# Kernel optimization log

Hardware: AMD Instinct MI355X
Metric: run time of the kernel (lower is better)

## Reference

```python
import jax, jax.numpy as jnp
import numpy as np

LN_EPS = 1e-5
NEG_SLOPE = 0.01

def layer_norm(h, gamma, beta):
    mu = jnp.mean(h, axis=-1, keepdims=True)
    var = jnp.var(h, axis=-1, keepdims=True)
    return (h - mu) * jax.lax.rsqrt(var + LN_EPS) * gamma + beta

def setup_inputs() -> dict:
    key = jax.random.key(0)
    ks = jax.random.split(key, 12)
    N, E = 50000, 600000
    D_NODE, D_EDGE, D_IN = 128, 64, 192  # D_IN = D_NODE + D_EDGE
    x = jax.random.normal(ks[0], (N, D_NODE), dtype=jnp.float32)
    edge_index = jax.random.randint(ks[1], (2, E), 0, N, dtype=jnp.int64)
    edge_attr = jax.random.normal(ks[2], (E, D_EDGE), dtype=jnp.float32)
    # mlp_before_agg: Linear(192->128) + LayerNorm + LeakyReLU
    W1 = jax.random.normal(ks[3], (D_IN, D_NODE), dtype=jnp.float32) / np.sqrt(D_IN)
    b1 = jnp.zeros((D_NODE,), dtype=jnp.float32)
    g1 = jnp.ones((D_NODE,), dtype=jnp.float32)
    be1 = jnp.zeros((D_NODE,), dtype=jnp.float32)
    # mlp_after_agg: Linear(128->128) + LayerNorm + LeakyReLU
    W2 = jax.random.normal(ks[4], (D_NODE, D_NODE), dtype=jnp.float32) / np.sqrt(D_NODE)
    b2 = jnp.zeros((D_NODE,), dtype=jnp.float32)
    g2 = jnp.ones((D_NODE,), dtype=jnp.float32)
    be2 = jnp.zeros((D_NODE,), dtype=jnp.float32)
    return {"x": x, "edge_index": edge_index, "edge_attr": edge_attr,
            "W1": W1, "b1": b1, "g1": g1, "be1": be1,
            "W2": W2, "b2": b2, "g2": g2, "be2": be2}

def reference(x, edge_index, edge_attr, W1, b1, g1, be1, W2, b2, g2, be2):
    N = x.shape[0]
    row, col = edge_index[0], edge_index[1]
    # 1. gather + concat: (E, D_NODE + D_EDGE)
    out = jnp.concatenate([x[row], edge_attr], axis=1)
    # 2. pre-agg MLP: Linear + LayerNorm + LeakyReLU
    out = jax.nn.leaky_relu(layer_norm(out @ W1 + b1, g1, be1), NEG_SLOPE)
    # 3. scatter-mean aggregate over destination nodes (empty segments -> 0)
    sums = jax.ops.segment_sum(out, col, num_segments=N)
    counts = jax.ops.segment_sum(jnp.ones((out.shape[0], 1), out.dtype), col, num_segments=N)
    out = sums / jnp.maximum(counts, 1.0)
    # 4. post-agg MLP + residual + activation
    out = jax.nn.leaky_relu(layer_norm(out @ W2 + b2, g2, be2), NEG_SLOPE)
    return jax.nn.leaky_relu(out + x, NEG_SLOPE)
```

## Files before the change

kernel.cpp:

```cpp
#include <hip/hip_runtime.h>

#define D_NODE 128
#define D_EDGE 64
#define D_IN   192
#define NEG    0.01f
#define LN_EPS 1e-5f

typedef short bf16x8 __attribute__((ext_vector_type(8)));
typedef float f32x4  __attribute__((ext_vector_type(4)));

__device__ __forceinline__ unsigned f2bf(float f) {
    unsigned u = __builtin_bit_cast(unsigned, f);
    return (u + 0x7FFFu + ((u >> 16) & 1u)) >> 16;
}
__device__ __forceinline__ unsigned pk2(float a, float b) {
    return f2bf(a) | (f2bf(b) << 16);
}
__device__ __forceinline__ float bf2f(unsigned short s) {
    unsigned u = ((unsigned)s) << 16;
    return __builtin_bit_cast(float, u);
}

__global__ void k_hist(const int* __restrict__ ei, int* __restrict__ hist, int E) {
    int i = blockIdx.x * blockDim.x + threadIdx.x;
    int stride = gridDim.x * blockDim.x;
    for (int e = i; e < E; e += stride) atomicAdd(&hist[ei[E + e]], 1);
}

__global__ __launch_bounds__(1024) void k_scanA(const int* __restrict__ hist,
                                                int* __restrict__ base,
                                                int* __restrict__ blockTot, int N) {
    __shared__ int wsum[16], woff[16];
    const int t = threadIdx.x, b = blockIdx.x;
    const int i = b * 1024 + t;
    const int lane = t & 63, w = t >> 6;
    int v = (i < N) ? hist[i] : 0;
    int x = v;
    #pragma unroll
    for (int d = 1; d < 64; d <<= 1) { int u = __shfl_up(x, d); if (lane >= d) x += u; }
    if (lane == 63) wsum[w] = x;
    __syncthreads();
    if (t < 16) {
        int y = wsum[t];
        #pragma unroll
        for (int d = 1; d < 16; d <<= 1) { int u = __shfl_up(y, d, 16); if (t >= d) y += u; }
        woff[t] = y - wsum[t];
    }
    __syncthreads();
    int incl = x + woff[w];
    if (i < N) base[i] = incl - v;
    if (t == 1023) blockTot[b] = incl;
}

__global__ void k_scanB(int* __restrict__ blockTot, int NB) {
    int t = threadIdx.x;
    int v = (t < NB) ? blockTot[t] : 0;
    int x = v;
    #pragma unroll
    for (int d = 1; d < 64; d <<= 1) { int u = __shfl_up(x, d); if (t >= d) x += u; }
    if (t < NB) blockTot[t] = x - v;
}

__global__ __launch_bounds__(1024) void k_scanC(int* __restrict__ base,
                                                const int* __restrict__ blockTot, int N) {
    int i = blockIdx.x * 1024 + threadIdx.x;
    if (i < N) base[i] += blockTot[blockIdx.x];
}

__global__ void k_bucket(const int* __restrict__ ei, int* __restrict__ base,
                         int* __restrict__ perm, int* __restrict__ srcrow,
                         int* __restrict__ dstcol, int E) {
    int i = blockIdx.x * blockDim.x + threadIdx.x;
    int stride = gridDim.x * blockDim.x;
    for (int e = i; e < E; e += stride) {
        int c = ei[E + e];
        int r = ei[e];
        int p = atomicAdd(&base[c], 1);
        perm[p]   = e;
        srcrow[p] = r;
        dstcol[p] = c;
    }
}

__global__ __launch_bounds__(256) void edge_mfma_seg(
    const float* __restrict__ x,
    const float* __restrict__ edge_attr,
    const int*   __restrict__ perm,
    const int*   __restrict__ srcrow,
    const int*   __restrict__ dstcol,
    const float* __restrict__ W1,
    const float* __restrict__ b1,
    const float* __restrict__ g1,
    const float* __restrict__ be1,
    float* __restrict__ sums,
    int E, int ntiles)
{
    __shared__ unsigned short h[64][200];
    __shared__ float rS [64][4], rS2[64][4];
    __shared__ int   scol[64];
    __shared__ unsigned long long maskSh;

    const int tid = threadIdx.x;
    const int w   = tid >> 6;
    const int l   = tid & 63;
    const int lm  = l & 15;
    const int q   = l >> 4;
    const int q8  = q * 8;

    bf16x8 Bfr[2][6];
    float  b1v[2], g1v[2], bev[2];
    #pragma unroll
    for (int c2 = 0; c2 < 2; ++c2) {
        const int n = (2 * w + c2) * 16 + lm;
        b1v[c2] = b1[n]; g1v[c2] = g1[n]; bev[c2] = be1[n];
        #pragma unroll
        for (int kt = 0; kt < 6; ++kt) {
            bf16x8 f;
            #pragma unroll
            for (int j = 0; j < 8; ++j)
                f[j] = (short)f2bf(W1[(kt * 32 + q8 + j) * 128 + n]);
            Bfr[c2][kt] = f;
        }
    }

    for (int tile = blockIdx.x; tile < ntiles; tile += gridDim.x) {
        const int e0 = tile * 64;

        {
            const int e  = tid >> 2;
            const int qq = tid & 3;
            const int ge = e0 + e;
            if (ge < E) {
                const int row = srcrow[ge];
                const int eid = perm[ge];
                const float4* xr = (const float4*)(x + (size_t)row * D_NODE);
                #pragma unroll
                for (int i = 0; i < 8; ++i) {
                    float4 v = xr[qq * 8 + i];
                    *(uint2*)&h[e][qq * 32 + i * 4] =
                        make_uint2(pk2(v.x, v.y), pk2(v.z, v.w));
                }
                const float4* ar = (const float4*)(edge_attr + (size_t)eid * D_EDGE);
                #pragma unroll
                for (int i = 0; i < 4; ++i) {
                    float4 v = ar[qq * 4 + i];
                    *(uint2*)&h[e][128 + qq * 16 + i * 4] =
                        make_uint2(pk2(v.x, v.y), pk2(v.z, v.w));
                }
            } else {
                #pragma unroll
                for (int i = 0; i < 8; ++i)
                    *(uint2*)&h[e][qq * 32 + i * 4] = make_uint2(0u, 0u);
                #pragma unroll
                for (int i = 0; i < 4; ++i)
                    *(uint2*)&h[e][128 + qq * 16 + i * 4] = make_uint2(0u, 0u);
            }
            if (tid < 64)
                scol[tid] = (e0 + tid < E) ? dstcol[e0 + tid] : -1;
        }
        __syncthreads();

        f32x4 acc[4][2];
        #pragma unroll
        for (int et = 0; et < 4; ++et)
            #pragma unroll
            for (int c2 = 0; c2 < 2; ++c2)
                acc[et][c2] = (f32x4){0.f, 0.f, 0.f, 0.f};

        #pragma unroll
        for (int et = 0; et < 4; ++et) {
            bf16x8 Afr[6];
            #pragma unroll
            for (int kt = 0; kt < 6; ++kt)
                Afr[kt] = *(const bf16x8*)&h[et * 16 + lm][kt * 32 + q8];
            #pragma unroll
            for (int c2 = 0; c2 < 2; ++c2)
                #pragma unroll
                for (int kt = 0; kt < 6; ++kt)
                    acc[et][c2] = __builtin_amdgcn_mfma_f32_16x16x32_bf16(
                        Afr[kt], Bfr[c2][kt], acc[et][c2], 0, 0, 0);
        }

        #pragma unroll
        for (int et = 0; et < 4; ++et) {
            #pragma unroll
            for (int r = 0; r < 4; ++r) {
                float v0 = acc[et][0][r] + b1v[0];
                float v1 = acc[et][1][r] + b1v[1];
                acc[et][0][r] = v0;
                acc[et][1][r] = v1;
                float s  = v0 + v1;
                float s2 = v0 * v0 + v1 * v1;
                #pragma unroll
                for (int off = 1; off < 16; off <<= 1) {
                    s  += __shfl_xor(s,  off, 16);
                    s2 += __shfl_xor(s2, off, 16);
                }
                if (lm == 0) {
                    const int em = et * 16 + q * 4 + r;
                    rS [em][w] = s;
                    rS2[em][w] = s2;
                }
            }
        }
        __syncthreads();

        if (tid < 64) {
            int me = scol[tid];
            int pv = (tid == 0) ? (me ^ 1) : scol[tid - 1];
            unsigned long long m = __ballot(me != pv);
            if (tid == 0) maskSh = m;
        }

        #pragma unroll
        for (int et = 0; et < 4; ++et) {
            #pragma unroll
            for (int r = 0; r < 4; ++r) {
                const int em = et * 16 + q * 4 + r;
                float4 p  = *(const float4*)&rS [em][0];
                float4 p2 = *(const float4*)&rS2[em][0];
                const float S    = (p.x  + p.y)  + (p.z  + p.w);
                const float S2   = (p2.x + p2.y) + (p2.z + p2.w);
                const float mu   = S * (1.f / 128.f);
                const float var  = S2 * (1.f / 128.f) - mu * mu;
                const float rstd = rsqrtf(var + LN_EPS);
                #pragma unroll
                for (int c2 = 0; c2 < 2; ++c2) {
                    float y = (acc[et][c2][r] - mu) * rstd * g1v[c2] + bev[c2];
                    y = (y > 0.f) ? y : NEG * y;
                    h[em][(2 * w + c2) * 16 + lm] = (unsigned short)f2bf(y);
                }
            }
        }
        __syncthreads();

        {
            const unsigned long long mask = maskSh;
            const int g  = tid >> 7;
            const int j  = tid & 127;
            const int lo = g * 32, hi = lo + 32;
            float s = 0.f;
            int rs = lo;
            for (int em = lo; em < hi; ++em) {
                s += bf2f(h[em][j]);
                const int nx = em + 1;
                const bool isEnd = (nx == hi) || ((mask >> nx) & 1ull);
                if (isEnd) {
                    const int dest = scol[em];
                    if (dest >= 0) {
                        const bool sg = (rs > 0) && ((mask >> rs) & 1ull);
                        const bool eg = (em < 63) && ((mask >> nx) & 1ull);
                        float* p = &sums[(size_t)dest * D_NODE + j];
                        if (sg && eg) *p = s;
                        else          atomicAdd(p, s);
                    }
                    s = 0.f; rs = nx;
                }
            }
        }
        __syncthreads();
    }
}

__global__ __launch_bounds__(256) void node_mfma(
    const float* __restrict__ sums,
    const int*   __restrict__ hist,
    const float* __restrict__ x,
    const float* __restrict__ W2,
    const float* __restrict__ b2,
    const float* __restrict__ g2,
    const float* __restrict__ be2,
    float* __restrict__ out,
    int N)
{
    __shared__ unsigned short h[64][136];
    __shared__ float rS [64][4], rS2[64][4];

    const int tid = threadIdx.x;
    const int w   = tid >> 6;
    const int l   = tid & 63;
    const int lm  = l & 15;
    const int q   = l >> 4;
    const int q8  = q * 8;

    bf16x8 Bfr[2][4];
    float  b2v[2], g2v[2], bev[2];
    #pragma unroll
    for (int c2 = 0; c2 < 2; ++c2) {
        const int n = (2 * w + c2) * 16 + lm;
        b2v[c2] = b2[n]; g2v[c2] = g2[n]; bev[c2] = be2[n];
        #pragma unroll
        for (int kt = 0; kt < 4; ++kt) {
            bf16x8 f;
            #pragma unroll
            for (int j = 0; j < 8; ++j)
                f[j] = (short)f2bf(W2[(kt * 32 + q8 + j) * 128 + n]);
            Bfr[c2][kt] = f;
        }
    }

    const int n0 = blockIdx.x * 64;

    {
        const int e  = tid >> 2;
        const int qq = tid & 3;
        const int gn = n0 + e;
        if (gn < N) {
            const int cnt = hist[gn];
            const float sc = (cnt > 0) ? 1.f / (float)cnt : 0.f;
            const float4* sr = (const float4*)(sums + (size_t)gn * D_NODE);
            #pragma unroll
            for (int i = 0; i < 8; ++i) {
                float4 v = sr[qq * 8 + i];
                *(uint2*)&h[e][qq * 32 + i * 4] =
                    make_uint2(pk2(v.x * sc, v.y * sc), pk2(v.z * sc, v.w * sc));
            }
        } else {
            #pragma unroll
            for (int i = 0; i < 8; ++i)
                *(uint2*)&h[e][qq * 32 + i * 4] = make_uint2(0u, 0u);
        }
    }
    __syncthreads();

    f32x4 acc[4][2];
    #pragma unroll
    for (int et = 0; et < 4; ++et)
        #pragma unroll
        for (int c2 = 0; c2 < 2; ++c2)
            acc[et][c2] = (f32x4){0.f, 0.f, 0.f, 0.f};

    #pragma unroll
    for (int et = 0; et < 4; ++et) {
        bf16x8 Afr[4];
        #pragma unroll
        for (int kt = 0; kt < 4; ++kt)
            Afr[kt] = *(const bf16x8*)&h[et * 16 + lm][kt * 32 + q8];
        #pragma unroll
        for (int c2 = 0; c2 < 2; ++c2)
            #pragma unroll
            for (int kt = 0; kt < 4; ++kt)
                acc[et][c2] = __builtin_amdgcn_mfma_f32_16x16x32_bf16(
                    Afr[kt], Bfr[c2][kt], acc[et][c2], 0, 0, 0);
    }

    #pragma unroll
    for (int et = 0; et < 4; ++et) {
        #pragma unroll
        for (int r = 0; r < 4; ++r) {
            float v0 = acc[et][0][r] + b2v[0];
            float v1 = acc[et][1][r] + b2v[1];
            acc[et][0][r] = v0;
            acc[et][1][r] = v1;
            float s  = v0 + v1;
            float s2 = v0 * v0 + v1 * v1;
            #pragma unroll
            for (int off = 1; off < 16; off <<= 1) {
                s  += __shfl_xor(s,  off, 16);
                s2 += __shfl_xor(s2, off, 16);
            }
            if (lm == 0) {
                const int em = et * 16 + q * 4 + r;
                rS [em][w] = s;
                rS2[em][w] = s2;
            }
        }
    }
    __syncthreads();

    #pragma unroll
    for (int et = 0; et < 4; ++et) {
        #pragma unroll
        for (int r = 0; r < 4; ++r) {
            const int em = et * 16 + q * 4 + r;
            const int gn = n0 + em;
            if (gn >= N) continue;
            float4 p  = *(const float4*)&rS [em][0];
            float4 p2 = *(const float4*)&rS2[em][0];
            const float S    = (p.x  + p.y)  + (p.z  + p.w);
            const float S2   = (p2.x + p2.y) + (p2.z + p2.w);
            const float mu   = S * (1.f / 128.f);
            const float var  = S2 * (1.f / 128.f) - mu * mu;
            const float rstd = rsqrtf(var + LN_EPS);
            #pragma unroll
            for (int c2 = 0; c2 < 2; ++c2) {
                const int col = (2 * w + c2) * 16 + lm;
                float y = (acc[et][c2][r] - mu) * rstd * g2v[c2] + bev[c2];
                y = (y > 0.f) ? y : NEG * y;
                float rr = y + x[(size_t)gn * D_NODE + col];
                rr = (rr > 0.f) ? rr : NEG * rr;
                out[(size_t)gn * D_NODE + col] = rr;
            }
        }
    }
}

extern "C" void kernel_launch(void* const* d_in, const int* in_sizes, int n_in,
                              void* d_out, int out_size, void* d_ws, size_t ws_size,
                              hipStream_t stream) {
    const float* x          = (const float*)d_in[0];
    const int*   edge_index = (const int*)  d_in[1];
    const float* edge_attr  = (const float*)d_in[2];
    const float* W1         = (const float*)d_in[3];
    const float* b1         = (const float*)d_in[4];
    const float* g1         = (const float*)d_in[5];
    const float* be1        = (const float*)d_in[6];
    const float* W2         = (const float*)d_in[7];
    const float* b2         = (const float*)d_in[8];
    const float* g2         = (const float*)d_in[9];
    const float* be2        = (const float*)d_in[10];

    const int N = in_sizes[0] / D_NODE;
    const int E = in_sizes[1] / 2;

    float* sums     = (float*)d_ws;
    int*   hist     = (int*)(sums + (size_t)N * D_NODE);
    int*   base     = hist + N;
    int*   blockTot = base + N;
    int*   perm     = blockTot + 64;
    int*   srcrow   = perm + E;
    int*   dstcol   = srcrow + E;

    hipMemsetAsync(d_ws, 0, ((size_t)N * D_NODE + (size_t)N) * sizeof(float), stream);

    k_hist<<<dim3(256), dim3(256), 0, stream>>>(edge_index, hist, E);
    const int NB = (N + 1023) / 1024;
    k_scanA<<<dim3(NB), dim3(1024), 0, stream>>>(hist, base, blockTot, N);
    k_scanB<<<dim3(1),  dim3(64),   0, stream>>>(blockTot, NB);
    k_scanC<<<dim3(NB), dim3(1024), 0, stream>>>(base, blockTot, N);
    k_bucket<<<dim3(256), dim3(256), 0, stream>>>(edge_index, base, perm, srcrow, dstcol, E);

    const int ntiles = (E + 63) / 64;
    const int grid   = ntiles < 1280 ? ntiles : 1280;
    edge_mfma_seg<<<dim3(grid), dim3(256), 0, stream>>>(
        x, edge_attr, perm, srcrow, dstcol, W1, b1, g1, be1, sums, E, ntiles);

    node_mfma<<<dim3((N + 63) / 64), dim3(256), 0, stream>>>(
        sums, hist, x, W2, b2, g2, be2, (float*)d_out, N);
}
```

Baseline: 509.7 us.

## Replace scan with atomic bucket allocation and pre-swizzle MFMA operand layout in LDS

The three-kernel prefix scan is replaced by a single atomic cursor allocator that gives each destination node a contiguous slot range, in arbitrary node order. The bucket kernel now writes only the permutation, and the edge kernel reads source and destination indices indirectly through edge_index. Gathered edge features are stored in LDS in an MFMA-fragment-ready layout so each lane loads one contiguous vector. The LayerNorm output is written transposed, so the segmented reduction reads contiguous per-column data, and that loop is fully unrolled. These changes cut launches and global index traffic, at the cost of extra indirect loads and narrower float2 global reads.

```diff
diff --git a/kernel.cpp b/kernel.cpp
--- a/kernel.cpp
+++ b/kernel.cpp
@@ -27,58 +27,19 @@
     for (int e = i; e < E; e += stride) atomicAdd(&hist[ei[E + e]], 1);
 }
 
-__global__ __launch_bounds__(1024) void k_scanA(const int* __restrict__ hist,
-                                                int* __restrict__ base,
-                                                int* __restrict__ blockTot, int N) {
-    __shared__ int wsum[16], woff[16];
-    const int t = threadIdx.x, b = blockIdx.x;
-    const int i = b * 1024 + t;
-    const int lane = t & 63, w = t >> 6;
-    int v = (i < N) ? hist[i] : 0;
-    int x = v;
-    #pragma unroll
-    for (int d = 1; d < 64; d <<= 1) { int u = __shfl_up(x, d); if (lane >= d) x += u; }
-    if (lane == 63) wsum[w] = x;
-    __syncthreads();
-    if (t < 16) {
-        int y = wsum[t];
-        #pragma unroll
-        for (int d = 1; d < 16; d <<= 1) { int u = __shfl_up(y, d, 16); if (t >= d) y += u; }
-        woff[t] = y - wsum[t];
-    }
-    __syncthreads();
-    int incl = x + woff[w];
-    if (i < N) base[i] = incl - v;
-    if (t == 1023) blockTot[b] = incl;
-}
-
-__global__ void k_scanB(int* __restrict__ blockTot, int NB) {
-    int t = threadIdx.x;
-    int v = (t < NB) ? blockTot[t] : 0;
-    int x = v;
-    #pragma unroll
-    for (int d = 1; d < 64; d <<= 1) { int u = __shfl_up(x, d); if (t >= d) x += u; }
-    if (t < NB) blockTot[t] = x - v;
-}
-
-__global__ __launch_bounds__(1024) void k_scanC(int* __restrict__ base,
-                                                const int* __restrict__ blockTot, int N) {
-    int i = blockIdx.x * 1024 + threadIdx.x;
-    if (i < N) base[i] += blockTot[blockIdx.x];
+__global__ void k_alloc(const int* __restrict__ hist, int* __restrict__ base,
+                        int* __restrict__ cursor, int N) {
+    int i = blockIdx.x * blockDim.x + threadIdx.x;
+    if (i < N) base[i] = atomicAdd(cursor, hist[i]);
 }
 
 __global__ void k_bucket(const int* __restrict__ ei, int* __restrict__ base,
-                         int* __restrict__ perm, int* __restrict__ srcrow,
-                         int* __restrict__ dstcol, int E) {
+                         int* __restrict__ perm, int E) {
     int i = blockIdx.x * blockDim.x + threadIdx.x;
     int stride = gridDim.x * blockDim.x;
     for (int e = i; e < E; e += stride) {
-        int c = ei[E + e];
-        int r = ei[e];
-        int p = atomicAdd(&base[c], 1);
-        perm[p]   = e;
-        srcrow[p] = r;
-        dstcol[p] = c;
+        int p = atomicAdd(&base[ei[E + e]], 1);
+        perm[p] = e;
     }
 }
 
@@ -86,8 +47,7 @@
     const float* __restrict__ x,
     const float* __restrict__ edge_attr,
     const int*   __restrict__ perm,
-    const int*   __restrict__ srcrow,
-    const int*   __restrict__ dstcol,
+    const int*   __restrict__ edge_index,
     const float* __restrict__ W1,
     const float* __restrict__ b1,
     const float* __restrict__ g1,
@@ -95,10 +55,11 @@
     float* __restrict__ sums,
     int E, int ntiles)
 {
-    __shared__ unsigned short h[64][200];
+    __shared__ unsigned short Af[12288];
     __shared__ float rS [64][4], rS2[64][4];
     __shared__ int   scol[64];
     __shared__ unsigned long long maskSh;
+    unsigned short* const yT = Af;
 
     const int tid = threadIdx.x;
     const int w   = tid >> 6;
@@ -127,36 +88,34 @@
         const int e0 = tile * 64;
 
         {
-            const int e  = tid >> 2;
-            const int qq = tid & 3;
-            const int ge = e0 + e;
+            const int e     = tid >> 2;
+            const int qq    = tid & 3;
+            const int et    = e >> 4;
+            const int elm   = e & 15;
+            const int ge    = e0 + e;
+            const int abase = et * 3072 + elm * 8 + qq * 2;
             if (ge < E) {
-                const int row = srcrow[ge];
                 const int eid = perm[ge];
-                const float4* xr = (const float4*)(x + (size_t)row * D_NODE);
+                const int row = edge_index[eid];
+                const float* xr = x + (size_t)row * D_NODE;
+                const float* ar = edge_attr + (size_t)eid * D_EDGE;
                 #pragma unroll
-                for (int i = 0; i < 8; ++i) {
-                    float4 v = xr[qq * 8 + i];
-                    *(uint2*)&h[e][qq * 32 + i * 4] =
-                        make_uint2(pk2(v.x, v.y), pk2(v.z, v.w));
-                }
-                const float4* ar = (const float4*)(edge_attr + (size_t)eid * D_EDGE);
-                #pragma unroll
-                for (int i = 0; i < 4; ++i) {
-                    float4 v = ar[qq * 4 + i];
-                    *(uint2*)&h[e][128 + qq * 16 + i * 4] =
-                        make_uint2(pk2(v.x, v.y), pk2(v.z, v.w));
+                for (int c = 0; c < 24; ++c) {
+                    const int k = c * 8 + qq * 2;
+                    float2 v;
+                    if (c < 16) v = *(const float2*)(xr + k);
+                    else        v = *(const float2*)(ar + (k - 128));
+                    *(unsigned*)&Af[abase + (c >> 2) * 512 + (c & 3) * 128] = pk2(v.x, v.y);
                 }
             } else {
                 #pragma unroll
-                for (int i = 0; i < 8; ++i)
-                    *(uint2*)&h[e][qq * 32 + i * 4] = make_uint2(0u, 0u);
-                #pragma unroll
-                for (int i = 0; i < 4; ++i)
-                    *(uint2*)&h[e][128 + qq * 16 + i * 4] = make_uint2(0u, 0u);
-            }
-            if (tid < 64)
-                scol[tid] = (e0 + tid < E) ? dstcol[e0 + tid] : -1;
+                for (int c = 0; c < 24; ++c)
+                    *(unsigned*)&Af[abase + (c >> 2) * 512 + (c & 3) * 128] = 0u;
+            }
+            if (tid < 64) {
+                const int ge2 = e0 + tid;
+                scol[tid] = (ge2 < E) ? edge_index[E + perm[ge2]] : -1;
+            }
         }
         __syncthreads();
 
@@ -172,7 +131,7 @@
             bf16x8 Afr[6];
             #pragma unroll
             for (int kt = 0; kt < 6; ++kt)
-                Afr[kt] = *(const bf16x8*)&h[et * 16 + lm][kt * 32 + q8];
+                Afr[kt] = *(const bf16x8*)&Af[et * 3072 + kt * 512 + l * 8];
             #pragma unroll
             for (int c2 = 0; c2 < 2; ++c2)
                 #pragma unroll
@@ -214,22 +173,32 @@
 
         #pragma unroll
         for (int et = 0; et < 4; ++et) {
+            float mur[4], rsr[4];
             #pragma unroll
             for (int r = 0; r < 4; ++r) {
                 const int em = et * 16 + q * 4 + r;
                 float4 p  = *(const float4*)&rS [em][0];
                 float4 p2 = *(const float4*)&rS2[em][0];
-                const float S    = (p.x  + p.y)  + (p.z  + p.w);
-                const float S2   = (p2.x + p2.y) + (p2.z + p2.w);
-                const float mu   = S * (1.f / 128.f);
-                const float var  = S2 * (1.f / 128.f) - mu * mu;
-                const float rstd = rsqrtf(var + LN_EPS);
+                const float S   = (p.x  + p.y)  + (p.z  + p.w);
+                const float S2  = (p2.x + p2.y) + (p2.z + p2.w);
+                const float mu  = S * (1.f / 128.f);
+                const float var = S2 * (1.f / 128.f) - mu * mu;
+                mur[r] = mu;
+                rsr[r] = rsqrtf(var + LN_EPS);
+            }
+            #pragma unroll
+            for (int c2 = 0; c2 < 2; ++c2) {
+                unsigned short pkv[4];
                 #pragma unroll
-                for (int c2 = 0; c2 < 2; ++c2) {
-                    float y = (acc[et][c2][r] - mu) * rstd * g1v[c2] + bev[c2];
+                for (int r = 0; r < 4; ++r) {
+                    float y = (acc[et][c2][r] - mur[r]) * rsr[r] * g1v[c2] + bev[c2];
                     y = (y > 0.f) ? y : NEG * y;
-                    h[em][(2 * w + c2) * 16 + lm] = (unsigned short)f2bf(y);
+                    pkv[r] = (unsigned short)f2bf(y);
                 }
+                const int col = (2 * w + c2) * 16 + lm;
+                *(uint2*)&yT[col * 68 + et * 16 + q * 4] =
+                    make_uint2((unsigned)pkv[0] | ((unsigned)pkv[1] << 16),
+                               (unsigned)pkv[2] | ((unsigned)pkv[3] << 16));
             }
         }
         __syncthreads();
@@ -238,13 +207,15 @@
             const unsigned long long mask = maskSh;
             const int g  = tid >> 7;
             const int j  = tid & 127;
-            const int lo = g * 32, hi = lo + 32;
+            const int lo = g * 32;
             float s = 0.f;
             int rs = lo;
-            for (int em = lo; em < hi; ++em) {
-                s += bf2f(h[em][j]);
+            #pragma unroll
+            for (int i = 0; i < 32; ++i) {
+                const int em = lo + i;
+                s += bf2f(yT[j * 68 + em]);
                 const int nx = em + 1;
-                const bool isEnd = (nx == hi) || ((mask >> nx) & 1ull);
+                const bool isEnd = (i == 31) || ((mask >> nx) & 1ull);
                 if (isEnd) {
                     const int dest = scol[em];
                     if (dest >= 0) {
@@ -413,27 +384,22 @@
     const int N = in_sizes[0] / D_NODE;
     const int E = in_sizes[1] / 2;
 
-    float* sums     = (float*)d_ws;
-    int*   hist     = (int*)(sums + (size_t)N * D_NODE);
-    int*   base     = hist + N;
-    int*   blockTot = base + N;
-    int*   perm     = blockTot + 64;
-    int*   srcrow   = perm + E;
-    int*   dstcol   = srcrow + E;
-
-    hipMemsetAsync(d_ws, 0, ((size_t)N * D_NODE + (size_t)N) * sizeof(float), stream);
-
-    k_hist<<<dim3(256), dim3(256), 0, stream>>>(edge_index, hist, E);
-    const int NB = (N + 1023) / 1024;
-    k_scanA<<<dim3(NB), dim3(1024), 0, stream>>>(hist, base, blockTot, N);
-    k_scanB<<<dim3(1),  dim3(64),   0, stream>>>(blockTot, NB);
-    k_scanC<<<dim3(NB), dim3(1024), 0, stream>>>(base, blockTot, N);
-    k_bucket<<<dim3(256), dim3(256), 0, stream>>>(edge_index, base, perm, srcrow, dstcol, E);
+    float* sums   = (float*)d_ws;
+    int*   hist   = (int*)(sums + (size_t)N * D_NODE);
+    int*   cursor = hist + N;
+    int*   base   = cursor + 1;
+    int*   perm   = base + N;
+
+    hipMemsetAsync(d_ws, 0, ((size_t)N * D_NODE + N + 1) * sizeof(float), stream);
+
+    k_hist  <<<dim3(512), dim3(256), 0, stream>>>(edge_index, hist, E);
+    k_alloc <<<dim3((N + 255) / 256), dim3(256), 0, stream>>>(hist, base, cursor, N);
+    k_bucket<<<dim3(512), dim3(256), 0, stream>>>(edge_index, base, perm, E);
 
     const int ntiles = (E + 63) / 64;
     const int grid   = ntiles < 1280 ? ntiles : 1280;
     edge_mfma_seg<<<dim3(grid), dim3(256), 0, stream>>>(
-        x, edge_attr, perm, srcrow, dstcol, W1, b1, g1, be1, sums, E, ntiles);
+        x, edge_attr, perm, edge_index, W1, b1, g1, be1, sums, E, ntiles);
 
     node_mfma<<<dim3((N + 63) / 64), dim3(256), 0, stream>>>(
         sums, hist, x, W2, b2, g2, be2, (float*)d_out, N);
```

Measured after the change: 655.3 us. 28.6% more time.
